# Kernel tuning notes

Measured on AMD Instinct MI355X. Metric: run time of the kernel, lower is better.

Reference implementation:

```python
import jax, jax.numpy as jnp
import numpy as np

N_QUBITS = 6
N_LAYERS = 4
N_ACTIONS = 4
PRE_DIM = 64
BATCH = 262144


def _cnot(state, ctrl, tgt):
    # state: (B, 2,...,2); flip target axis on the control=1 slice
    ca, ta = 1 + ctrl, 1 + tgt
    s0 = jnp.take(state, 0, axis=ca)
    s1 = jnp.take(state, 1, axis=ca)
    ta_in = ta if ta < ca else ta - 1
    s1 = jnp.flip(s1, axis=ta_in)
    return jnp.stack([s0, s1], axis=ca)


def _ry_batched(state, angles_q, q):
    # angles_q: (B,) per-sample RY angle on qubit q (AngleEmbedding)
    h = angles_q * 0.5
    c, s = jnp.cos(h), jnp.sin(h)
    R = jnp.stack([jnp.stack([c, -s], -1), jnp.stack([s, c], -1)], -2)  # (B,2,2)
    st = jnp.moveaxis(state, 1 + q, -1)
    st = jnp.einsum('b...i,bji->b...j', st, R)
    return jnp.moveaxis(st, -1, 1 + q)


def _ry_scalar(state, theta, q):
    h = theta * 0.5
    c, s = jnp.cos(h), jnp.sin(h)
    R = jnp.stack([jnp.stack([c, -s]), jnp.stack([s, c])])  # (2,2)
    st = jnp.moveaxis(state, 1 + q, -1)
    st = st @ R.T  # new_j = sum_i R[j,i] amp_i
    return jnp.moveaxis(st, -1, 1 + q)


def _circuit(xp, qw):
    # xp: (B, n_qubits) angles; qw: (n_layers, n_qubits)
    B = xp.shape[0]
    state = jnp.zeros((B,) + (2,) * N_QUBITS, xp.dtype)
    state = state.at[(slice(None),) + (0,) * N_QUBITS].set(1.0)
    for q in range(N_QUBITS):
        state = _ry_batched(state, xp[:, q], q)
    for l in range(N_LAYERS):
        for i in range(N_QUBITS):
            state = _cnot(state, i, (i + 1) % N_QUBITS)
        for i in range(N_QUBITS):
            state = _ry_scalar(state, qw[l, i], i)
    probs = state * state  # RY/CNOT are real; state stays real
    all_axes = tuple(range(1, N_QUBITS + 1))
    zs = []
    for q in range(N_QUBITS):
        p = jnp.sum(probs, axis=tuple(a for a in all_axes if a != 1 + q))  # (B,2)
        zs.append(p[:, 0] - p[:, 1])
    return jnp.stack(zs, -1)  # (B, n_qubits)


def setup_inputs() -> dict:
    key = jax.random.key(0)
    ks = jax.random.split(key, 10)
    x = jax.random.normal(ks[0], (BATCH, N_QUBITS), jnp.float32)
    sc = 1.0 / np.sqrt(N_QUBITS)
    W1 = jax.random.uniform(ks[1], (PRE_DIM, N_QUBITS), jnp.float32, -sc, sc)
    b1 = jax.random.uniform(ks[2], (PRE_DIM,), jnp.float32, -sc, sc)
    sc2 = 1.0 / np.sqrt(PRE_DIM)
    W2 = jax.random.uniform(ks[3], (N_QUBITS, PRE_DIM), jnp.float32, -sc2, sc2)
    b2 = jax.random.uniform(ks[4], (N_QUBITS,), jnp.float32, -sc2, sc2)
    qw = jax.random.uniform(ks[5], (N_LAYERS, N_QUBITS), jnp.float32, 0.0, 2.0 * np.pi)
    Wp = jax.random.uniform(ks[6], (N_ACTIONS, N_QUBITS), jnp.float32, -sc, sc)
    bp = jax.random.uniform(ks[7], (N_ACTIONS,), jnp.float32, -sc, sc)
    Wv = jax.random.uniform(ks[8], (1, N_QUBITS), jnp.float32, -sc, sc)
    bv = jax.random.uniform(ks[9], (1,), jnp.float32, -sc, sc)
    return {"x": x, "W1": W1, "b1": b1, "W2": W2, "b2": b2, "qw": qw,
            "Wp": Wp, "bp": bp, "Wv": Wv, "bv": bv}


def reference(x, W1, b1, W2, b2, qw, Wp, bp, Wv, bv):
    h = jax.nn.relu(x @ W1.T + b1)
    xp = jax.nn.relu(h @ W2.T + b2)          # (B, n_qubits)
    qout = _circuit(xp, qw)                   # (B, n_qubits)
    policy = jax.nn.softmax(qout @ Wp.T + bp, axis=-1)
    value = (qout @ Wv.T + bv)[:, 0]
    return policy, value
```

## Files before the change

kernel.cpp:

```cpp
#include <hip/hip_runtime.h>
#include <math.h>


#define NQ 6
#define NL 4
#define NA 4
#define PD 64

typedef float v2 __attribute__((ext_vector_type(2)));

static __device__ __forceinline__ v2 mk2(float a, float b) { v2 r; r.x = a; r.y = b; return r; }
static __device__ __forceinline__ v2 pkfma(v2 a, v2 b, v2 c) { return __builtin_elementwise_fma(a, b, c); }

static __device__ __forceinline__ float dppx1(float v) {
    int i = __builtin_bit_cast(int, v);
    i = __builtin_amdgcn_mov_dpp(i, 0xB1, 0xF, 0xF, true);
    return __builtin_bit_cast(float, i);
}

__global__ __launch_bounds__(256) void mlp_kernel(
    const float* __restrict__ x,
    const float* __restrict__ W1,
    const float* __restrict__ b1,
    const float* __restrict__ W2,
    const float* __restrict__ b2,
    const float* __restrict__ qw,
    float* __restrict__ ws,
    int B)
{
    const int s = blockIdx.x * blockDim.x + threadIdx.x;

    if (blockIdx.x == 0 && threadIdx.x < NL * NQ) {
        const int l = threadIdx.x / NQ, i = threadIdx.x % NQ;
        const float hh0 = 0.5f * qw[l * NQ + i];
        float* dst = ws + l * 16;
        if (i == 0) {
            dst[0] = cosf(hh0);
            dst[1] = sinf(hh0);
        } else if (i == 5) {
            dst[10] = cosf(hh0);
            dst[11] = sinf(hh0);
        } else {
            const float hh = (hh0 > 1.5707963f) ? (hh0 - 3.14159265358979f) : hh0;
            const float sh = sinf(hh), ch = cosf(hh);
            dst[2 * i]     = -sh / (1.0f + ch);
            dst[2 * i + 1] = sh;
        }
    }
    if (s >= B) return;

    const v2* xv = reinterpret_cast<const v2*>(x + (size_t)s * NQ);
    const v2 x01 = xv[0], x23 = xv[1], x45 = xv[2];

    const v2* W1v = reinterpret_cast<const v2*>(W1);
    const v2* W2v = reinterpret_cast<const v2*>(W2);

    v2 xpa[NQ];
#pragma unroll
    for (int i = 0; i < NQ; ++i) xpa[i] = mk2(b2[i], 0.0f);
#pragma unroll
    for (int k2 = 0; k2 < PD / 2; ++k2) {
        float hu[2];
#pragma unroll
        for (int u = 0; u < 2; ++u) {
            const int j = 2 * k2 + u;
            v2 acc = mk2(b1[j], 0.0f);
            acc = pkfma(x01, W1v[j * 3 + 0], acc);
            acc = pkfma(x23, W1v[j * 3 + 1], acc);
            acc = pkfma(x45, W1v[j * 3 + 2], acc);
            hu[u] = fmaxf(acc.x + acc.y, 0.0f);
        }
        const v2 hv = mk2(hu[0], hu[1]);
#pragma unroll
        for (int i = 0; i < NQ; ++i)
            xpa[i] = pkfma(hv, W2v[i * (PD / 2) + k2], xpa[i]);
    }

    float cs[12];
#pragma unroll
    for (int i = 0; i < NQ; ++i) {
        const float xp = fmaxf(xpa[i].x + xpa[i].y, 0.0f);
        float sh, ch;
        __sincosf(0.5f * xp, &sh, &ch);
        cs[2 * i] = ch; cs[2 * i + 1] = sh;
    }
    float4* o = reinterpret_cast<float4*>(ws + 256) + (size_t)s * 3;
#pragma unroll
    for (int i = 0; i < 3; ++i)
        o[i] = make_float4(cs[4 * i], cs[4 * i + 1], cs[4 * i + 2], cs[4 * i + 3]);
}

__global__ __launch_bounds__(256) void qpolicy_kernel(
    const float* __restrict__ ws,
    const float* __restrict__ Wp,
    const float* __restrict__ bp,
    const float* __restrict__ Wv,
    const float* __restrict__ bv,
    float* __restrict__ out,
    int B)
{
    const int t = blockIdx.x * blockDim.x + threadIdx.x;
    const int s = t >> 1;
    const bool podd = (t & 1) != 0;

    const v2* csv = reinterpret_cast<const v2*>(ws + 256) + (size_t)s * 6;
    v2 cs[6];
#pragma unroll
    for (int q = 0; q < 6; ++q) cs[q] = csv[q];

    const float g0 = podd ? cs[0].y : cs[0].x;
    const v2 cs1f = podd ? __builtin_shufflevector(cs[1], cs[1], 1, 0) : cs[1];
    const v2 e1 = mk2(g0, g0) * cs1f;
    v2 e2[2], e3[4], e4[8], st[16];
    e2[0] = mk2(e1.x, e1.x) * cs[2];
    e2[1] = mk2(e1.y, e1.y) * cs[2];
#pragma unroll
    for (int k = 0; k < 2; ++k) {
        e3[2 * k]     = mk2(e2[k].x, e2[k].x) * cs[3];
        e3[2 * k + 1] = mk2(e2[k].y, e2[k].y) * cs[3];
    }
#pragma unroll
    for (int k = 0; k < 4; ++k) {
        e4[2 * k]     = mk2(e3[k].x, e3[k].x) * cs[4];
        e4[2 * k + 1] = mk2(e3[k].y, e3[k].y) * cs[4];
    }
#pragma unroll
    for (int k = 0; k < 8; ++k) {
        st[2 * k]     = mk2(e4[k].x, e4[k].x) * cs[5];
        st[2 * k + 1] = mk2(e4[k].y, e4[k].y) * cs[5];
    }

#pragma unroll
    for (int l = 0; l < NL; ++l) {
        const float* cst = ws + l * 16;

        if (l > 0) {
#pragma unroll
            for (int j = 0; j < 8; ++j) {
                const v2 a = st[j], b = st[j | 8];
                st[j]     = podd ? b : a;
                st[j | 8] = podd ? a : b;
            }
        }
#pragma unroll
        for (int j = 0; j < 16; ++j)
            if ((j & 8) && !(j & 4)) { v2 tm = st[j]; st[j] = st[j | 4]; st[j | 4] = tm; }
#pragma unroll
        for (int j = 0; j < 16; ++j)
            if ((j & 4) && !(j & 2)) { v2 tm = st[j]; st[j] = st[j | 2]; st[j | 2] = tm; }
#pragma unroll
        for (int j = 0; j < 16; ++j)
            if ((j & 2) && !(j & 1)) { v2 tm = st[j]; st[j] = st[j | 1]; st[j | 1] = tm; }
#pragma unroll
        for (int j = 0; j < 16; ++j)
            if (j & 1) st[j] = __builtin_shufflevector(st[j], st[j], 1, 0);

        {
            const float c0 = cst[0], s0 = cst[1];
            const float ssg = podd ? s0 : -s0;
            const v2 KA = mk2(c0, ssg);
            const v2 KB = mk2(ssg, c0);
#pragma unroll
            for (int j = 0; j < 16; ++j) {
                const float dx = dppx1(st[j].x);
                const float dy = dppx1(st[j].y);
                st[j] = pkfma(KB, mk2(dx, dy), KA * st[j]);
            }
        }

#pragma unroll
        for (int i = 1; i <= 4; ++i) {
            const int m = 1 << (4 - i);
            const v2 vnt = mk2(cst[2 * i], cst[2 * i]);
            const v2 vs  = mk2(cst[2 * i + 1], cst[2 * i + 1]);
#pragma unroll
            for (int j = 0; j < 16; ++j) {
                if (!(j & m)) {
                    v2 a = st[j], b = st[j | m];
                    a = pkfma(vnt, b, a);
                    b = pkfma(vs, a, b);
                    a = pkfma(vnt, b, a);
                    st[j] = a; st[j | m] = b;
                }
            }
        }
        {
            const float c5 = cst[10], s5 = cst[11];
            const v2 ms  = mk2(-s5, s5);
            const v2 vc5 = mk2(c5, c5);
#pragma unroll
            for (int j = 0; j < 16; ++j) {
                const v2 sw = __builtin_shufflevector(st[j], st[j], 1, 0);
                st[j] = pkfma(ms, sw, st[j] * vc5);
            }
        }
    }

    v2 asq[16];
#pragma unroll
    for (int j = 0; j < 16; ++j) asq[j] = st[j] * st[j];

    v2 s1a = asq[0];
#pragma unroll
    for (int j = 1; j < 8; ++j) s1a += asq[j];
    v2 c8[8];
#pragma unroll
    for (int j = 0; j < 8; ++j) c8[j] = asq[j] + asq[j | 8];
    v2 c4[4];
#pragma unroll
    for (int j = 0; j < 4; ++j) c4[j] = c8[j] + c8[j | 4];
    const v2 s2a = (c8[0] + c8[1]) + (c8[2] + c8[3]);
    v2 c2[2];
    c2[0] = c4[0] + c4[2];
    c2[1] = c4[1] + c4[3];
    const v2 s3a = c4[0] + c4[1];
    const v2 s4a = c2[0];
    const v2 ta  = c2[0] + c2[1];

    const float Tl  = ta.x + ta.y;
    const float S5l = ta.x;
    const float S1l = s1a.x + s1a.y;
    const float S2l = s2a.x + s2a.y;
    const float S3l = s3a.x + s3a.y;
    const float S4l = s4a.x + s4a.y;

    const float To = dppx1(Tl);
    const float T  = Tl + To;
    const float S0 = podd ? To : Tl;
    const float S1 = S1l + dppx1(S1l);
    const float S2 = S2l + dppx1(S2l);
    const float S3 = S3l + dppx1(S3l);
    const float S4 = S4l + dppx1(S4l);
    const float S5 = S5l + dppx1(S5l);

    float z[NQ];
    z[0] = fmaf(2.0f, S0, -T);
    z[1] = fmaf(2.0f, S1, -T);
    z[2] = fmaf(2.0f, S2, -T);
    z[3] = fmaf(2.0f, S3, -T);
    z[4] = fmaf(2.0f, S4, -T);
    z[5] = fmaf(2.0f, S5, -T);

    float logits[NA];
#pragma unroll
    for (int aidx = 0; aidx < NA; ++aidx) {
        float acc = bp[aidx];
#pragma unroll
        for (int q = 0; q < NQ; ++q) acc = fmaf(z[q], Wp[aidx * NQ + q], acc);
        logits[aidx] = acc;
    }
    float m = logits[0];
#pragma unroll
    for (int aidx = 1; aidx < NA; ++aidx) m = fmaxf(m, logits[aidx]);
    float e[NA];
    float esum = 0.0f;
#pragma unroll
    for (int aidx = 0; aidx < NA; ++aidx) { e[aidx] = __expf(logits[aidx] - m); esum += e[aidx]; }
    const float inv = 1.0f / esum;

    float4 pol;
    pol.x = e[0] * inv; pol.y = e[1] * inv; pol.z = e[2] * inv; pol.w = e[3] * inv;

    float v = bv[0];
#pragma unroll
    for (int q = 0; q < NQ; ++q) v = fmaf(z[q], Wv[q], v);

    if (!podd) {
        reinterpret_cast<float4*>(out)[s] = pol;
        out[(size_t)B * NA + s] = v;
    }
}

extern "C" void kernel_launch(void* const* d_in, const int* in_sizes, int n_in,
                              void* d_out, int out_size, void* d_ws, size_t ws_size,
                              hipStream_t stream) {
    const float* x  = (const float*)d_in[0];
    const float* W1 = (const float*)d_in[1];
    const float* b1 = (const float*)d_in[2];
    const float* W2 = (const float*)d_in[3];
    const float* b2 = (const float*)d_in[4];
    const float* qw = (const float*)d_in[5];
    const float* Wp = (const float*)d_in[6];
    const float* bp = (const float*)d_in[7];
    const float* Wv = (const float*)d_in[8];
    const float* bv = (const float*)d_in[9];
    float* out = (float*)d_out;
    float* ws  = (float*)d_ws;

    const int B = in_sizes[0] / NQ;

    hipLaunchKernelGGL(mlp_kernel, dim3((B + 255) / 256), dim3(256), 0, stream,
                       x, W1, b1, W2, b2, qw, ws, B);

    hipLaunchKernelGGL(qpolicy_kernel, dim3((2 * B + 255) / 256), dim3(256), 0, stream,
                       ws, Wp, bp, Wv, bv, out, B);
}
```

Baseline: 106.0 us.

## Fuse MLP and quantum-circuit kernels into one launch with shared-memory handoff

Merges the MLP/angle kernel and the circuit/policy kernel into a single kernel. Half the threads of each block compute the MLP and sincos for 128 samples and write them to shared memory, while a few others compute the per-layer rotation constants into shared memory. After a barrier, all 256 threads run the two-threads-per-sample circuit. This removes the global workspace round trip and one launch, but leaves half the block idle during the MLP phase and adds a block-level sync.

```diff
diff --git a/kernel.cpp b/kernel.cpp
--- a/kernel.cpp
+++ b/kernel.cpp
@@ -18,22 +18,64 @@
     return __builtin_bit_cast(float, i);
 }
 
-__global__ __launch_bounds__(256) void mlp_kernel(
+__global__ __launch_bounds__(256) void qpolicy_fused(
     const float* __restrict__ x,
     const float* __restrict__ W1,
     const float* __restrict__ b1,
     const float* __restrict__ W2,
     const float* __restrict__ b2,
     const float* __restrict__ qw,
-    float* __restrict__ ws,
+    const float* __restrict__ Wp,
+    const float* __restrict__ bp,
+    const float* __restrict__ Wv,
+    const float* __restrict__ bv,
+    float* __restrict__ out,
     int B)
 {
-    const int s = blockIdx.x * blockDim.x + threadIdx.x;
-
-    if (blockIdx.x == 0 && threadIdx.x < NL * NQ) {
-        const int l = threadIdx.x / NQ, i = threadIdx.x % NQ;
+    __shared__ float cst[NL * 16];
+    __shared__ v2 csh[NQ][128];
+
+    const int tid = threadIdx.x;
+
+    if (tid < 128) {
+        const int s = blockIdx.x * 128 + tid;
+        const v2* xv = reinterpret_cast<const v2*>(x + (size_t)s * NQ);
+        const v2 x01 = xv[0], x23 = xv[1], x45 = xv[2];
+
+        const v2* W1v = reinterpret_cast<const v2*>(W1);
+        const v2* W2v = reinterpret_cast<const v2*>(W2);
+
+        v2 xpa[NQ];
+#pragma unroll
+        for (int i = 0; i < NQ; ++i) xpa[i] = mk2(b2[i], 0.0f);
+#pragma unroll
+        for (int k2 = 0; k2 < PD / 2; ++k2) {
+            float hu[2];
+#pragma unroll
+            for (int u = 0; u < 2; ++u) {
+                const int j = 2 * k2 + u;
+                v2 acc = mk2(b1[j], 0.0f);
+                acc = pkfma(x01, W1v[j * 3 + 0], acc);
+                acc = pkfma(x23, W1v[j * 3 + 1], acc);
+                acc = pkfma(x45, W1v[j * 3 + 2], acc);
+                hu[u] = fmaxf(acc.x + acc.y, 0.0f);
+            }
+            const v2 hv = mk2(hu[0], hu[1]);
+#pragma unroll
+            for (int i = 0; i < NQ; ++i)
+                xpa[i] = pkfma(hv, W2v[i * (PD / 2) + k2], xpa[i]);
+        }
+#pragma unroll
+        for (int i = 0; i < NQ; ++i) {
+            const float xp = fmaxf(xpa[i].x + xpa[i].y, 0.0f);
+            float sh, ch;
+            __sincosf(0.5f * xp, &sh, &ch);
+            csh[i][tid] = mk2(ch, sh);
+        }
+    } else if (tid < 128 + NL * NQ) {
+        const int k = tid - 128, l = k / NQ, i = k - l * NQ;
         const float hh0 = 0.5f * qw[l * NQ + i];
-        float* dst = ws + l * 16;
+        float* dst = cst + l * 16;
         if (i == 0) {
             dst[0] = cosf(hh0);
             dst[1] = sinf(hh0);
@@ -47,66 +89,15 @@
             dst[2 * i + 1] = sh;
         }
     }
-    if (s >= B) return;
-
-    const v2* xv = reinterpret_cast<const v2*>(x + (size_t)s * NQ);
-    const v2 x01 = xv[0], x23 = xv[1], x45 = xv[2];
-
-    const v2* W1v = reinterpret_cast<const v2*>(W1);
-    const v2* W2v = reinterpret_cast<const v2*>(W2);
-
-    v2 xpa[NQ];
-#pragma unroll
-    for (int i = 0; i < NQ; ++i) xpa[i] = mk2(b2[i], 0.0f);
-#pragma unroll
-    for (int k2 = 0; k2 < PD / 2; ++k2) {
-        float hu[2];
-#pragma unroll
-        for (int u = 0; u < 2; ++u) {
-            const int j = 2 * k2 + u;
-            v2 acc = mk2(b1[j], 0.0f);
-            acc = pkfma(x01, W1v[j * 3 + 0], acc);
-            acc = pkfma(x23, W1v[j * 3 + 1], acc);
-            acc = pkfma(x45, W1v[j * 3 + 2], acc);
-            hu[u] = fmaxf(acc.x + acc.y, 0.0f);
-        }
-        const v2 hv = mk2(hu[0], hu[1]);
-#pragma unroll
-        for (int i = 0; i < NQ; ++i)
-            xpa[i] = pkfma(hv, W2v[i * (PD / 2) + k2], xpa[i]);
-    }
-
-    float cs[12];
-#pragma unroll
-    for (int i = 0; i < NQ; ++i) {
-        const float xp = fmaxf(xpa[i].x + xpa[i].y, 0.0f);
-        float sh, ch;
-        __sincosf(0.5f * xp, &sh, &ch);
-        cs[2 * i] = ch; cs[2 * i + 1] = sh;
-    }
-    float4* o = reinterpret_cast<float4*>(ws + 256) + (size_t)s * 3;
-#pragma unroll
-    for (int i = 0; i < 3; ++i)
-        o[i] = make_float4(cs[4 * i], cs[4 * i + 1], cs[4 * i + 2], cs[4 * i + 3]);
-}
-
-__global__ __launch_bounds__(256) void qpolicy_kernel(
-    const float* __restrict__ ws,
-    const float* __restrict__ Wp,
-    const float* __restrict__ bp,
-    const float* __restrict__ Wv,
-    const float* __restrict__ bv,
-    float* __restrict__ out,
-    int B)
-{
-    const int t = blockIdx.x * blockDim.x + threadIdx.x;
-    const int s = t >> 1;
-    const bool podd = (t & 1) != 0;
-
-    const v2* csv = reinterpret_cast<const v2*>(ws + 256) + (size_t)s * 6;
-    v2 cs[6];
-#pragma unroll
-    for (int q = 0; q < 6; ++q) cs[q] = csv[q];
+    __syncthreads();
+
+    const int sl = tid >> 1;
+    const int s  = blockIdx.x * 128 + sl;
+    const bool podd = (tid & 1) != 0;
+
+    v2 cs[NQ];
+#pragma unroll
+    for (int q = 0; q < NQ; ++q) cs[q] = csh[q][sl];
 
     const float g0 = podd ? cs[0].y : cs[0].x;
     const v2 cs1f = podd ? __builtin_shufflevector(cs[1], cs[1], 1, 0) : cs[1];
@@ -132,7 +123,9 @@
 
 #pragma unroll
     for (int l = 0; l < NL; ++l) {
-        const float* cst = ws + l * 16;
+        float lc[12];
+#pragma unroll
+        for (int k = 0; k < 12; ++k) lc[k] = cst[l * 16 + k];
 
         if (l > 0) {
 #pragma unroll
@@ -156,7 +149,7 @@
             if (j & 1) st[j] = __builtin_shufflevector(st[j], st[j], 1, 0);
 
         {
-            const float c0 = cst[0], s0 = cst[1];
+            const float c0 = lc[0], s0 = lc[1];
             const float ssg = podd ? s0 : -s0;
             const v2 KA = mk2(c0, ssg);
             const v2 KB = mk2(ssg, c0);
@@ -171,8 +164,8 @@
 #pragma unroll
         for (int i = 1; i <= 4; ++i) {
             const int m = 1 << (4 - i);
-            const v2 vnt = mk2(cst[2 * i], cst[2 * i]);
-            const v2 vs  = mk2(cst[2 * i + 1], cst[2 * i + 1]);
+            const v2 vnt = mk2(lc[2 * i], lc[2 * i]);
+            const v2 vs  = mk2(lc[2 * i + 1], lc[2 * i + 1]);
 #pragma unroll
             for (int j = 0; j < 16; ++j) {
                 if (!(j & m)) {
@@ -185,7 +178,7 @@
             }
         }
         {
-            const float c5 = cst[10], s5 = cst[11];
+            const float c5 = lc[10], s5 = lc[11];
             const v2 ms  = mk2(-s5, s5);
             const v2 vc5 = mk2(c5, c5);
 #pragma unroll
@@ -285,13 +278,10 @@
     const float* Wv = (const float*)d_in[8];
     const float* bv = (const float*)d_in[9];
     float* out = (float*)d_out;
-    float* ws  = (float*)d_ws;
+    (void)d_ws; (void)ws_size;
 
     const int B = in_sizes[0] / NQ;
 
-    hipLaunchKernelGGL(mlp_kernel, dim3((B + 255) / 256), dim3(256), 0, stream,
-                       x, W1, b1, W2, b2, qw, ws, B);
-
-    hipLaunchKernelGGL(qpolicy_kernel, dim3((2 * B + 255) / 256), dim3(256), 0, stream,
-                       ws, Wp, bp, Wv, bv, out, B);
+    hipLaunchKernelGGL(qpolicy_fused, dim3((2 * B + 255) / 256), dim3(256), 0, stream,
+                       x, W1, b1, W2, b2, qw, Wp, bp, Wv, bv, out, B);
 }
```

Result: faster. 101.4 us (-4.4%).
